# Kernel tuning notes

Measured on AMD Instinct MI355X. Metric: run time of the kernel, lower is better.

Reference implementation:

```python
import jax, jax.numpy as jnp
import numpy as np

B, C, H, W = 4, 32, 120, 160
NH = 8  # num_heads; head_dim = W // NH = 20; seq N = C*H = 3840


def setup_inputs() -> dict:
    key = jax.random.key(0)
    ks = jax.random.split(key, 7)
    s = 1.0 / np.sqrt(W)
    u = lambda k, shape: jax.random.uniform(k, shape, jnp.float32, -s, s)
    return {
        "x": jax.random.normal(ks[0], (B, C, H, W), jnp.float32),
        "Wq": u(ks[1], (W, W)), "bq": u(ks[2], (W,)),
        "Wk": u(ks[3], (W, W)), "bk": u(ks[4], (W,)),
        "Wv": u(ks[5], (W, W)), "bv": u(ks[6], (W,)),
    }


def reference(x, Wq, bq, Wk, bk, Wv, bv):
    b, c, h, w = x.shape
    hd = w // NH          # head_dim
    n = c * h             # effective sequence length (raw contiguous view)
    # Linear acts on last dim (W); torch weight is (out,in) -> x @ W.T + b
    q = (x @ Wq.T + bq).reshape(b, NH, hd, n)
    k = (x @ Wk.T + bk).reshape(b, NH, hd, n)
    v = (x @ Wv.T + bv).reshape(b, NH, hd, n)
    # energy = q^T k : (b,nh,n,n); NOTE: unscaled, as in the source
    energy = jnp.einsum('bhdn,bhdm->bhnm', q, k)
    attn = jax.nn.softmax(energy, axis=-1)
    # out = v @ attn : (b,nh,hd,n)
    out = jnp.einsum('bhdm,bhmn->bhdn', v, attn)
    # permute(0,2,1,3) then view(B,C,H,W)
    return out.transpose(0, 2, 1, 3).reshape(b, c, h, w)
```

## Files before the change

### kernel.cpp

```cpp
#include <hip/hip_runtime.h>
#include <hip/hip_bf16.h>
#include <math.h>

#define BB   4
#define CC   32
#define HH   120
#define WW   160
#define NH_  8
#define HD   20
#define HDP  32
#define NN   3840
#define ROWS 3840
#define NBH  32
#define LOG2E 1.44269504088896f

typedef float f32x4 __attribute__((ext_vector_type(4)));
typedef short s16x8 __attribute__((ext_vector_type(8)));
typedef short s16x4 __attribute__((ext_vector_type(4)));

static __device__ __forceinline__ unsigned short f2bf(float x) {
    return __builtin_bit_cast(unsigned short, __float2bfloat16(x));
}
static __device__ __forceinline__ float bf2f(unsigned short u) {
    unsigned v = ((unsigned)u) << 16;
    return __builtin_bit_cast(float, v);
}
static __device__ __forceinline__ float exp2fast(float x) {
#if defined(__has_builtin) && __has_builtin(__builtin_amdgcn_exp2f)
    return __builtin_amdgcn_exp2f(x);
#else
    float r; asm("v_exp_f32 %0, %1" : "=v"(r) : "v"(x)); return r;
#endif
}

static __device__ __forceinline__ s16x4 exp4_pack(f32x4 e) {
    unsigned u0 = __builtin_bit_cast(unsigned, exp2fast(e[0])) + 0x8000u;
    unsigned u1 = __builtin_bit_cast(unsigned, exp2fast(e[1])) + 0x8000u;
    unsigned u2 = __builtin_bit_cast(unsigned, exp2fast(e[2])) + 0x8000u;
    unsigned u3 = __builtin_bit_cast(unsigned, exp2fast(e[3])) + 0x8000u;
    uint2 w;
#if defined(__has_builtin) && __has_builtin(__builtin_amdgcn_perm)
    w.x = __builtin_amdgcn_perm(u1, u0, 0x07060302u);
    w.y = __builtin_amdgcn_perm(u3, u2, 0x07060302u);
#else
    w.x = (u0 >> 16) | (u1 & 0xffff0000u);
    w.y = (u2 >> 16) | (u3 & 0xffff0000u);
#endif
    return __builtin_bit_cast(s16x4, w);
}

static __device__ __forceinline__ f32x4 mfma32(s16x8 a, s16x8 b, f32x4 c) {
    return __builtin_amdgcn_mfma_f32_16x16x32_bf16(a, b, c, 0, 0, 0);
}
static __device__ __forceinline__ s16x8 cat44(s16x4 a, s16x4 b) {
    s16x8 r;
    r[0]=a[0]; r[1]=a[1]; r[2]=a[2]; r[3]=a[3];
    r[4]=b[0]; r[5]=b[1]; r[6]=b[2]; r[7]=b[3];
    return r;
}

__global__ __launch_bounds__(256)
void wprep_kernel(const float* __restrict__ Wq, const float* __restrict__ Wk,
                  const float* __restrict__ Wv,
                  unsigned short* __restrict__ wqb, unsigned short* __restrict__ wkb,
                  unsigned short* __restrict__ wvb)
{
    int i = blockIdx.x*256 + threadIdx.x;
    if (i < WW*WW) {
        wqb[i] = f2bf(Wq[i] * LOG2E);
        wkb[i] = f2bf(Wk[i]);
        wvb[i] = f2bf(Wv[i]);
    }
}

__global__ __launch_bounds__(256)
void proj_mfma_kernel(const float* __restrict__ x,
                      const unsigned short* __restrict__ wqb,
                      const unsigned short* __restrict__ wkb,
                      const unsigned short* __restrict__ wvb,
                      const float* __restrict__ bq, const float* __restrict__ bk,
                      const float* __restrict__ bv,
                      unsigned short* __restrict__ qt, unsigned short* __restrict__ kt,
                      unsigned short* __restrict__ vb)
{
    const int tid  = threadIdx.x;
    const int wv   = tid >> 6;
    const int lane = tid & 63;
    const int g = lane >> 4, c = lane & 15;
    const int r0 = blockIdx.x*64 + wv*16;

    s16x8 A[5];
    const float* xrow = x + (size_t)(r0 + c)*WW;
    #pragma unroll
    for (int s = 0; s < 5; ++s) {
        float4 v0 = *(const float4*)(xrow + s*32 + g*8);
        float4 v1 = *(const float4*)(xrow + s*32 + g*8 + 4);
        s16x8 a;
        a[0]=(short)f2bf(v0.x); a[1]=(short)f2bf(v0.y);
        a[2]=(short)f2bf(v0.z); a[3]=(short)f2bf(v0.w);
        a[4]=(short)f2bf(v1.x); a[5]=(short)f2bf(v1.y);
        a[6]=(short)f2bf(v1.z); a[7]=(short)f2bf(v1.w);
        A[s] = a;
    }

    size_t baseqk[4], basev[4];
    #pragma unroll
    for (int rr = 0; rr < 4; ++rr) {
        int R  = r0 + g*4 + rr;
        int b  = R / ROWS;
        int r  = R % ROWS;
        int nh = r / 480;
        int rm = r % 480;
        int d  = rm / 24;
        int n1 = rm % 24;
        int bh = b*NH_ + nh;
        baseqk[rr] = ((size_t)bh*NN + n1*160)*HDP + d;
        basev[rr]  = ((size_t)bh*HD + d)*NN + n1*160;
    }

    const f32x4 zero4 = {0.f, 0.f, 0.f, 0.f};
    for (int nt = 0; nt < 10; ++nt) {
        const size_t wbase = (size_t)(nt*16 + c)*WW;
        f32x4 aq = zero4, ak = zero4, av = zero4;
        #pragma unroll
        for (int s = 0; s < 5; ++s) {
            s16x8 Bq = *(const s16x8*)(wqb + wbase + s*32 + g*8);
            aq = mfma32(A[s], Bq, aq);
            s16x8 Bk = *(const s16x8*)(wkb + wbase + s*32 + g*8);
            ak = mfma32(A[s], Bk, ak);
            s16x8 Bv = *(const s16x8*)(wvb + wbase + s*32 + g*8);
            av = mfma32(A[s], Bv, av);
        }
        const int o = nt*16 + c;
        const float bqv = bq[o]*LOG2E, bkv = bk[o], bvv = bv[o];
        #pragma unroll
        for (int rr = 0; rr < 4; ++rr) {
            qt[baseqk[rr] + (size_t)o*HDP] = f2bf(aq[rr] + bqv);
            kt[baseqk[rr] + (size_t)o*HDP] = f2bf(ak[rr] + bkv);
            vb[basev[rr] + o]              = f2bf(av[rr] + bvv);
        }
    }
}

__global__ __launch_bounds__(256, 4)
void zinv_kernel(const unsigned short* __restrict__ qt,
                 const unsigned short* __restrict__ kt,
                 float* __restrict__ zinv)
{
    __shared__ float zred[4][64];
    const int blk  = ((int)blockIdx.x & 7) * (NBH*(NN/64)/8) + ((int)blockIdx.x >> 3);
    const int bh   = blk / (NN/64);
    const int m0   = (blk % (NN/64)) * 64;
    const int tid  = threadIdx.x;
    const int wv   = tid >> 6;
    const int lane = tid & 63;
    const int g = lane >> 4, c = lane & 15;

    s16x8 qa[4];
    #pragma unroll
    for (int ms = 0; ms < 4; ++ms)
        qa[ms] = *(const s16x8*)(qt + ((size_t)bh*NN + m0 + ms*16 + c)*HDP + g*8);

    const f32x4 zero4 = {0.f, 0.f, 0.f, 0.f};
    f32x4 z[4];
    #pragma unroll
    for (int ms = 0; ms < 4; ++ms) z[ms] = zero4;

    const unsigned short* kbase = kt + (size_t)bh*NN*HDP;
    const int nbeg = wv * (NN/4);
    const int nend = nbeg + NN/4;

    s16x8 kb0 = *(const s16x8*)(kbase + (size_t)(nbeg +      c)*HDP + g*8);
    s16x8 kb1 = *(const s16x8*)(kbase + (size_t)(nbeg + 16 + c)*HDP + g*8);

    for (int n = nbeg; n < nend - 32; n += 32) {
        s16x8 nk0 = *(const s16x8*)(kbase + (size_t)(n + 32 +      c)*HDP + g*8);
        s16x8 nk1 = *(const s16x8*)(kbase + (size_t)(n + 48 +      c)*HDP + g*8);
        #pragma unroll
        for (int ms = 0; ms < 4; ++ms) {
            f32x4 e0 = mfma32(qa[ms], kb0, zero4);
            f32x4 e1 = mfma32(qa[ms], kb1, zero4);
            #pragma unroll
            for (int rr = 0; rr < 4; ++rr)
                z[ms][rr] += exp2fast(e0[rr]) + exp2fast(e1[rr]);
        }
        kb0 = nk0; kb1 = nk1;
    }
    #pragma unroll
    for (int ms = 0; ms < 4; ++ms) {
        f32x4 e0 = mfma32(qa[ms], kb0, zero4);
        f32x4 e1 = mfma32(qa[ms], kb1, zero4);
        #pragma unroll
        for (int rr = 0; rr < 4; ++rr)
            z[ms][rr] += exp2fast(e0[rr]) + exp2fast(e1[rr]);
    }

    #pragma unroll
    for (int ms = 0; ms < 4; ++ms) {
        #pragma unroll
        for (int rr = 0; rr < 4; ++rr) {
            float v = z[ms][rr];
            v += __shfl_xor(v, 1);
            v += __shfl_xor(v, 2);
            v += __shfl_xor(v, 4);
            v += __shfl_xor(v, 8);
            if (c == 0) zred[wv][ms*16 + g*4 + rr] = v;
        }
    }
    __syncthreads();
    if (tid < 64) {
        float s = zred[0][tid] + zred[1][tid] + zred[2][tid] + zred[3][tid];
        zinv[(size_t)bh*NN + m0 + tid] = 1.0f / s;
    }
}

__global__ __launch_bounds__(256)
void vz_kernel(const unsigned short* __restrict__ vb,
               const float* __restrict__ zinv,
               unsigned short* __restrict__ vzt)
{
    size_t idx = (size_t)blockIdx.x*256 + threadIdx.x;
    int dp = (int)(idx % HDP);
    size_t t = idx / HDP;
    int q  = (int)(t % (NN/4));
    int bh = (int)(t / (NN/4));
    float v0=0.f, v1=0.f, v2=0.f, v3=0.f;
    if (dp < HD) {
        const unsigned short* src = vb + ((size_t)bh*HD + dp)*NN + q*4;
        const float* zi = zinv + (size_t)bh*NN + q*4;
        v0 = bf2f(src[0])*zi[0];
        v1 = bf2f(src[1])*zi[1];
        v2 = bf2f(src[2])*zi[2];
        v3 = bf2f(src[3])*zi[3];
    }
    s16x4 o;
    o[0]=(short)f2bf(v0); o[1]=(short)f2bf(v1);
    o[2]=(short)f2bf(v2); o[3]=(short)f2bf(v3);
    *(s16x4*)(vzt + (size_t)bh*HDP*NN + (size_t)q*(HDP*4) + dp*4) = o;
}

__global__ __launch_bounds__(256, 3)
void attn_out_kernel(const unsigned short* __restrict__ qt,
                     const unsigned short* __restrict__ kt,
                     const unsigned short* __restrict__ vzt,
                     float* __restrict__ y)
{
    __shared__ float red[3][32][64];
    const int blk  = ((int)blockIdx.x & 7) * (NBH*(NN/64)/8) + ((int)blockIdx.x >> 3);
    const int bh   = blk / (NN/64);
    const int n0   = (blk % (NN/64)) * 64;
    const int tid  = threadIdx.x;
    const int wv   = tid >> 6;
    const int lane = tid & 63;
    const int g = lane >> 4, c = lane & 15;
    const int b = bh >> 3, nh = bh & 7;

    const f32x4 zero4 = {0.f, 0.f, 0.f, 0.f};
    const unsigned short* qb  = qt  + (size_t)bh*NN*HDP;
    const unsigned short* kbp = kt  + (size_t)bh*NN*HDP;
    const unsigned short* vp  = vzt + (size_t)bh*HDP*NN;

    s16x8 kb[4];
    #pragma unroll
    for (int ns = 0; ns < 4; ++ns)
        kb[ns] = *(const s16x8*)(kbp + ((size_t)(n0 + ns*16 + c))*HDP + g*8);

    f32x4 acc[2][4];
    #pragma unroll
    for (int ds = 0; ds < 2; ++ds)
        #pragma unroll
        for (int ns = 0; ns < 4; ++ns) acc[ds][ns] = zero4;

    const int mbeg = wv * (NN/4);
    const int mend = mbeg + NN/4;

    s16x8 qa[4];
    s16x4 va[2][4];
    #pragma unroll
    for (int j = 0; j < 4; ++j)
        qa[j] = *(const s16x8*)(qb + ((size_t)(mbeg + j*16 + c))*HDP + g*8);
    #pragma unroll
    for (int ds = 0; ds < 2; ++ds)
        #pragma unroll
        for (int j = 0; j < 4; ++j)
            va[ds][j] = *(const s16x4*)(vp + (size_t)((mbeg >> 2) + j*4 + g)*(HDP*4)
                                           + (ds*16 + c)*4);

    for (int m0 = mbeg; m0 < mend - 64; m0 += 64) {
        const int m1 = m0 + 64;
        s16x8 nqa[4];
        s16x4 nva[2][4];
        #pragma unroll
        for (int j = 0; j < 4; ++j)
            nqa[j] = *(const s16x8*)(qb + ((size_t)(m1 + j*16 + c))*HDP + g*8);
        #pragma unroll
        for (int ds = 0; ds < 2; ++ds)
            #pragma unroll
            for (int j = 0; j < 4; ++j)
                nva[ds][j] = *(const s16x4*)(vp + (size_t)((m1 >> 2) + j*4 + g)*(HDP*4)
                                                + (ds*16 + c)*4);

        #pragma unroll
        for (int ns = 0; ns < 4; ++ns) {
            f32x4 e0 = mfma32(qa[0], kb[ns], zero4);
            f32x4 e1 = mfma32(qa[1], kb[ns], zero4);
            f32x4 e2 = mfma32(qa[2], kb[ns], zero4);
            f32x4 e3 = mfma32(qa[3], kb[ns], zero4);
            s16x8 P01 = cat44(exp4_pack(e0), exp4_pack(e1));
            s16x8 P23 = cat44(exp4_pack(e2), exp4_pack(e3));
            acc[0][ns] = mfma32(cat44(va[0][0], va[0][1]), P01, acc[0][ns]);
            acc[0][ns] = mfma32(cat44(va[0][2], va[0][3]), P23, acc[0][ns]);
            acc[1][ns] = mfma32(cat44(va[1][0], va[1][1]), P01, acc[1][ns]);
            acc[1][ns] = mfma32(cat44(va[1][2], va[1][3]), P23, acc[1][ns]);
        }
        #pragma unroll
        for (int j = 0; j < 4; ++j) qa[j] = nqa[j];
        #pragma unroll
        for (int ds = 0; ds < 2; ++ds)
            #pragma unroll
            for (int j = 0; j < 4; ++j) va[ds][j] = nva[ds][j];
    }
    #pragma unroll
    for (int ns = 0; ns < 4; ++ns) {
        f32x4 e0 = mfma32(qa[0], kb[ns], zero4);
        f32x4 e1 = mfma32(qa[1], kb[ns], zero4);
        f32x4 e2 = mfma32(qa[2], kb[ns], zero4);
        f32x4 e3 = mfma32(qa[3], kb[ns], zero4);
        s16x8 P01 = cat44(exp4_pack(e0), exp4_pack(e1));
        s16x8 P23 = cat44(exp4_pack(e2), exp4_pack(e3));
        acc[0][ns] = mfma32(cat44(va[0][0], va[0][1]), P01, acc[0][ns]);
        acc[0][ns] = mfma32(cat44(va[0][2], va[0][3]), P23, acc[0][ns]);
        acc[1][ns] = mfma32(cat44(va[1][0], va[1][1]), P01, acc[1][ns]);
        acc[1][ns] = mfma32(cat44(va[1][2], va[1][3]), P23, acc[1][ns]);
    }

    float* af = (float*)acc;
    if (wv > 0) {
        #pragma unroll
        for (int j = 0; j < 32; ++j) red[wv-1][j][lane] = af[j];
    }
    __syncthreads();
    if (wv == 0) {
        #pragma unroll
        for (int j = 0; j < 32; ++j)
            af[j] += red[0][j][lane] + red[1][j][lane] + red[2][j][lane];
        float* yb = y + (size_t)b * CC * HH * WW;
        #pragma unroll
        for (int ds = 0; ds < 2; ++ds) {
            #pragma unroll
            for (int ns = 0; ns < 4; ++ns) {
                #pragma unroll
                for (int rr = 0; rr < 4; ++rr) {
                    int dd = ds*16 + g*4 + rr;
                    if (dd < HD)
                        yb[((size_t)(dd*NH_ + nh))*NN + n0 + ns*16 + c] = acc[ds][ns][rr];
                }
            }
        }
    }
}

extern "C" void kernel_launch(void* const* d_in, const int* in_sizes, int n_in,
                              void* d_out, int out_size, void* d_ws, size_t ws_size,
                              hipStream_t stream)
{
    const float* x  = (const float*)d_in[0];
    const float* Wq = (const float*)d_in[1];
    const float* bq = (const float*)d_in[2];
    const float* Wk = (const float*)d_in[3];
    const float* bk = (const float*)d_in[4];
    const float* Wv = (const float*)d_in[5];
    const float* bv = (const float*)d_in[6];
    float* y = (float*)d_out;

    const size_t QT_E = (size_t)NBH * NN * HDP;
    unsigned short* qt  = (unsigned short*)d_ws;
    unsigned short* kt  = qt + QT_E;
    unsigned short* vb  = kt + QT_E;
    unsigned short* vzt = vb + (size_t)NBH * HD * NN;
    float*          zinv = (float*)(vzt + QT_E);
    unsigned short* wqb = (unsigned short*)(zinv + (size_t)NBH*NN);
    unsigned short* wkb = wqb + WW*WW;
    unsigned short* wvb = wkb + WW*WW;

    hipMemsetAsync(qt, 0, 2 * QT_E * sizeof(unsigned short), stream);

    wprep_kernel<<<dim3((WW*WW + 255)/256), dim3(256), 0, stream>>>(
        Wq, Wk, Wv, wqb, wkb, wvb);
    proj_mfma_kernel<<<dim3(BB*ROWS/64), dim3(256), 0, stream>>>(
        x, wqb, wkb, wvb, bq, bk, bv, qt, kt, vb);
    zinv_kernel<<<dim3(NBH*(NN/64)), dim3(256), 0, stream>>>(qt, kt, zinv);
    vz_kernel<<<dim3((NBH*(NN/4)*HDP)/256), dim3(256), 0, stream>>>(vb, zinv, vzt);
    attn_out_kernel<<<dim3(NBH*(NN/64)), dim3(256), 0, stream>>>(qt, kt, vzt, y);
}
```

Baseline: 190.1 us.

## Fold softmax normalizer into QK dot via padded bf16 slots, drop vz pass

```diff
diff --git a/kernel.cpp b/kernel.cpp
--- a/kernel.cpp
+++ b/kernel.cpp
@@ -74,6 +74,16 @@
 }
 
 __global__ __launch_bounds__(256)
+void ones_kernel(unsigned short* __restrict__ kt)
+{
+    int i = blockIdx.x*256 + threadIdx.x;
+    if (i < NBH*NN) {
+        kt[(size_t)i*HDP + 30] = 0x3F80;
+        kt[(size_t)i*HDP + 31] = 0x3F80;
+    }
+}
+
+__global__ __launch_bounds__(256)
 void proj_mfma_kernel(const float* __restrict__ x,
                       const unsigned short* __restrict__ wqb,
                       const unsigned short* __restrict__ wkb,
@@ -81,7 +91,7 @@
                       const float* __restrict__ bq, const float* __restrict__ bk,
                       const float* __restrict__ bv,
                       unsigned short* __restrict__ qt, unsigned short* __restrict__ kt,
-                      unsigned short* __restrict__ vb)
+                      unsigned short* __restrict__ vt)
 {
     const int tid  = threadIdx.x;
     const int wv   = tid >> 6;
@@ -103,7 +113,7 @@
         A[s] = a;
     }
 
-    size_t baseqk[4], basev[4];
+    size_t baseqk[4], vq0[4];
     #pragma unroll
     for (int rr = 0; rr < 4; ++rr) {
         int R  = r0 + g*4 + rr;
@@ -115,7 +125,7 @@
         int n1 = rm % 24;
         int bh = b*NH_ + nh;
         baseqk[rr] = ((size_t)bh*NN + n1*160)*HDP + d;
-        basev[rr]  = ((size_t)bh*HD + d)*NN + n1*160;
+        vq0[rr]    = (size_t)bh*NN*HDP + (size_t)(n1*40)*(HDP*4) + (size_t)d*4;
     }
 
     const f32x4 zero4 = {0.f, 0.f, 0.f, 0.f};
@@ -137,15 +147,14 @@
         for (int rr = 0; rr < 4; ++rr) {
             qt[baseqk[rr] + (size_t)o*HDP] = f2bf(aq[rr] + bqv);
             kt[baseqk[rr] + (size_t)o*HDP] = f2bf(ak[rr] + bkv);
-            vb[basev[rr] + o]              = f2bf(av[rr] + bvv);
+            vt[vq0[rr] + (size_t)(o >> 2)*(HDP*4) + (o & 3)] = f2bf(av[rr] + bvv);
         }
     }
 }
 
 __global__ __launch_bounds__(256, 4)
-void zinv_kernel(const unsigned short* __restrict__ qt,
-                 const unsigned short* __restrict__ kt,
-                 float* __restrict__ zinv)
+void zinv_kernel(unsigned short* __restrict__ qt,
+                 const unsigned short* __restrict__ kt)
 {
     __shared__ float zred[4][64];
     const int blk  = ((int)blockIdx.x & 7) * (NBH*(NN/64)/8) + ((int)blockIdx.x >> 3);
@@ -210,39 +219,19 @@
     __syncthreads();
     if (tid < 64) {
         float s = zred[0][tid] + zred[1][tid] + zred[2][tid] + zred[3][tid];
-        zinv[(size_t)bh*NN + m0 + tid] = 1.0f / s;
-    }
-}
-
-__global__ __launch_bounds__(256)
-void vz_kernel(const unsigned short* __restrict__ vb,
-               const float* __restrict__ zinv,
-               unsigned short* __restrict__ vzt)
-{
-    size_t idx = (size_t)blockIdx.x*256 + threadIdx.x;
-    int dp = (int)(idx % HDP);
-    size_t t = idx / HDP;
-    int q  = (int)(t % (NN/4));
-    int bh = (int)(t / (NN/4));
-    float v0=0.f, v1=0.f, v2=0.f, v3=0.f;
-    if (dp < HD) {
-        const unsigned short* src = vb + ((size_t)bh*HD + dp)*NN + q*4;
-        const float* zi = zinv + (size_t)bh*NN + q*4;
-        v0 = bf2f(src[0])*zi[0];
-        v1 = bf2f(src[1])*zi[1];
-        v2 = bf2f(src[2])*zi[2];
-        v3 = bf2f(src[3])*zi[3];
-    }
-    s16x4 o;
-    o[0]=(short)f2bf(v0); o[1]=(short)f2bf(v1);
-    o[2]=(short)f2bf(v2); o[3]=(short)f2bf(v3);
-    *(s16x4*)(vzt + (size_t)bh*HDP*NN + (size_t)q*(HDP*4) + dp*4) = o;
+        float lzf = -__log2f(s);
+        unsigned short hi = f2bf(lzf);
+        unsigned short lo = f2bf(lzf - bf2f(hi));
+        size_t qoff = ((size_t)bh*NN + m0 + tid)*HDP;
+        qt[qoff + 30] = hi;
+        qt[qoff + 31] = lo;
+    }
 }
 
 __global__ __launch_bounds__(256, 3)
 void attn_out_kernel(const unsigned short* __restrict__ qt,
                      const unsigned short* __restrict__ kt,
-                     const unsigned short* __restrict__ vzt,
+                     const unsigned short* __restrict__ vt,
                      float* __restrict__ y)
 {
     __shared__ float red[3][32][64];
@@ -256,9 +245,9 @@
     const int b = bh >> 3, nh = bh & 7;
 
     const f32x4 zero4 = {0.f, 0.f, 0.f, 0.f};
-    const unsigned short* qb  = qt  + (size_t)bh*NN*HDP;
-    const unsigned short* kbp = kt  + (size_t)bh*NN*HDP;
-    const unsigned short* vp  = vzt + (size_t)bh*HDP*NN;
+    const unsigned short* qb  = qt + (size_t)bh*NN*HDP;
+    const unsigned short* kbp = kt + (size_t)bh*NN*HDP;
+    const unsigned short* vp  = vt + (size_t)bh*HDP*NN;
 
     s16x8 kb[4];
     #pragma unroll
@@ -376,20 +365,18 @@
     const size_t QT_E = (size_t)NBH * NN * HDP;
     unsigned short* qt  = (unsigned short*)d_ws;
     unsigned short* kt  = qt + QT_E;
-    unsigned short* vb  = kt + QT_E;
-    unsigned short* vzt = vb + (size_t)NBH * HD * NN;
-    float*          zinv = (float*)(vzt + QT_E);
-    unsigned short* wqb = (unsigned short*)(zinv + (size_t)NBH*NN);
+    unsigned short* vt  = kt + QT_E;
+    unsigned short* wqb = vt + QT_E;
     unsigned short* wkb = wqb + WW*WW;
     unsigned short* wvb = wkb + WW*WW;
 
-    hipMemsetAsync(qt, 0, 2 * QT_E * sizeof(unsigned short), stream);
+    hipMemsetAsync(qt, 0, 3 * QT_E * sizeof(unsigned short), stream);
 
     wprep_kernel<<<dim3((WW*WW + 255)/256), dim3(256), 0, stream>>>(
         Wq, Wk, Wv, wqb, wkb, wvb);
+    ones_kernel<<<dim3((NBH*NN)/256), dim3(256), 0, stream>>>(kt);
     proj_mfma_kernel<<<dim3(BB*ROWS/64), dim3(256), 0, stream>>>(
-        x, wqb, wkb, wvb, bq, bk, bv, qt, kt, vb);
-    zinv_kernel<<<dim3(NBH*(NN/64)), dim3(256), 0, stream>>>(qt, kt, zinv);
-    vz_kernel<<<dim3((NBH*(NN/4)*HDP)/256), dim3(256), 0, stream>>>(vb, zinv, vzt);
-    attn_out_kernel<<<dim3(NBH*(NN/64)), dim3(256), 0, stream>>>(qt, kt, vzt, y);
-}
+        x, wqb, wkb, wvb, bq, bk, bv, qt, kt, vt);
+    zinv_kernel<<<dim3(NBH*(NN/64)), dim3(256), 0, stream>>>(qt, kt);
+    attn_out_kernel<<<dim3(NBH*(NN/64)), dim3(256), 0, stream>>>(qt, kt, vt, y);
+}
```

Result: slower. 194.6 us (+2.4%).
